# Kernel tuning notes

Hardware: AMD Instinct MI355X
Metric: run time of the kernel (lower is better)

## Reference

```python
import jax, jax.numpy as jnp
import numpy as np

D_MODEL = 1024
D_FF = 4096


def _layernorm(x, gamma, beta, eps=1e-5):
    mu = jnp.mean(x, axis=-1, keepdims=True)
    var = jnp.var(x, axis=-1, keepdims=True)
    return (x - mu) * jax.lax.rsqrt(var + eps) * gamma + beta


def setup_inputs() -> dict:
    key = jax.random.key(0)
    ks = jax.random.split(key, 7)
    B, S = 4, 2048
    src = jax.random.normal(ks[0], (B, S, D_MODEL), dtype=jnp.float32)
    gamma1 = jnp.ones((D_MODEL,), jnp.float32)
    beta1 = jnp.zeros((D_MODEL,), jnp.float32)
    gamma2 = jnp.ones((D_MODEL,), jnp.float32)
    beta2 = jnp.zeros((D_MODEL,), jnp.float32)
    w1 = jax.random.normal(ks[1], (D_MODEL, D_FF), jnp.float32) * (1.0 / np.sqrt(D_MODEL))
    b1 = jnp.zeros((D_FF,), jnp.float32)
    w2 = jax.random.normal(ks[2], (D_FF, D_MODEL), jnp.float32) * (1.0 / np.sqrt(D_FF))
    b2 = jnp.zeros((D_MODEL,), jnp.float32)
    return {"src": src, "gamma1": gamma1, "beta1": beta1,
            "gamma2": gamma2, "beta2": beta2,
            "w1": w1, "b1": b1, "w2": w2, "b2": b2}


def reference(src, gamma1, beta1, gamma2, beta2, w1, b1, w2, b2):
    # Pre-LN self-attention (single head, Q=K=V=norm_x, no projections)
    norm_x = _layernorm(src, gamma1, beta1)
    dim_k = norm_x.shape[-1]
    scores = jnp.einsum('bqd,bkd->bqk', norm_x, norm_x) / jnp.sqrt(jnp.float32(dim_k))
    weights = jax.nn.softmax(scores, axis=-1)
    attn = jnp.einsum('bqk,bkd->bqd', weights, norm_x)
    x = src + attn  # dropout p=0 -> identity
    # Pre-LN FFN
    h = _layernorm(x, gamma2, beta2)
    h = jax.nn.gelu(h @ w1 + b1, approximate=False)
    h = h @ w2 + b2
    return h + x
```

## Files before the change

### kernel.cpp

```cpp
#include <hip/hip_runtime.h>
#include <hip/hip_bf16.h>
#include <math.h>

typedef __attribute__((ext_vector_type(8))) short s8vec;
typedef __attribute__((ext_vector_type(16))) float f32x16;
typedef __attribute__((ext_vector_type(4))) unsigned short us4;

__device__ __forceinline__ unsigned short f2bf(float f) {
  unsigned u = __float_as_uint(f);
  u = (u + 0x7fffu + ((u >> 16) & 1u)) >> 16;
  return (unsigned short)u;
}
__device__ __forceinline__ float bf2f(unsigned short u) {
  return __uint_as_float(((unsigned)u) << 16);
}

__device__ __forceinline__ float fast_gelu(float t) {
  float t2 = t * t;
  float u = t * (1.59576912f + 0.07135481f * t2);
  float e = __expf(-u);
  return t * __frcp_rn(1.0f + e);
}

__device__ __forceinline__ void async_ld16(const unsigned short* g, unsigned short* l) {
  __builtin_amdgcn_global_load_lds(
      (__attribute__((address_space(1))) void*)g,
      (__attribute__((address_space(3))) void*)l, 16, 0, 0);
}

template <int EPI>
__global__ __launch_bounds__(256) void gemm_nt(
    const unsigned short* __restrict__ A, const unsigned short* __restrict__ B,
    float* __restrict__ outF, unsigned short* __restrict__ outB,
    const float* __restrict__ bias, const float* __restrict__ res,
    int M, int N, int K,
    long long bA, long long bB, long long bO, long long bR, float scale)
{
  __shared__ __align__(16) unsigned short As[128 * 64];
  __shared__ __align__(16) unsigned short Bs[128 * 64];

  const int tid = threadIdx.x;
  const int w = tid >> 6;
  const int l = tid & 63;
  const int z = blockIdx.z;

  A += (size_t)z * bA;
  B += (size_t)z * bB;

  const size_t tileM = (size_t)blockIdx.y * 128;
  const size_t tileN = (size_t)blockIdx.x * 128;

  const int sRow = l >> 3;
  const unsigned short* aP[4];
  const unsigned short* bP[4];
#pragma unroll
  for (int i = 0; i < 4; ++i) {
    const int c = (l & 7) ^ sRow ^ i;
    aP[i] = A + (tileM + (w << 5) + (i << 3) + sRow) * (size_t)K + (c << 3);
    bP[i] = B + (tileN + (w << 5) + (i << 3) + sRow) * (size_t)K + (c << 3);
  }
  unsigned short* ldsA = &As[(w << 5) * 64];
  unsigned short* ldsB = &Bs[(w << 5) * 64];

  const int wm = (w >> 1) << 6;
  const int wn = (w & 1) << 6;
  const int fr = l & 31;
  const int fq = l >> 5;
  const int swz = (l & 7) ^ ((l >> 3) & 3);
  const int aRow = (wm + fr) * 64;
  const int bRow = (wn + fr) * 64;

  f32x16 acc[2][2] = {};

  for (int k0 = 0; k0 < K; k0 += 64) {
    __syncthreads();
#pragma unroll
    for (int i = 0; i < 4; ++i) {
      async_ld16(aP[i] + k0, ldsA + (i << 3) * 64);
      async_ld16(bP[i] + k0, ldsB + (i << 3) * 64);
    }
    __syncthreads();

#pragma unroll
    for (int s = 0; s < 4; ++s) {
      const int p = ((s << 1) + fq) ^ swz;
      s8vec af[2], bf[2];
#pragma unroll
      for (int i = 0; i < 2; ++i)
        af[i] = *(const s8vec*)&As[aRow + (i << 11) + (p << 3)];
#pragma unroll
      for (int j = 0; j < 2; ++j)
        bf[j] = *(const s8vec*)&Bs[bRow + (j << 11) + (p << 3)];
#pragma unroll
      for (int i = 0; i < 2; ++i)
#pragma unroll
        for (int j = 0; j < 2; ++j)
          acc[i][j] = __builtin_amdgcn_mfma_f32_32x32x16_bf16(af[i], bf[j], acc[i][j], 0, 0, 0);
    }
  }

  float* oF = outF + (size_t)z * bO;
  unsigned short* oB = outB + (size_t)z * bO;
  const float* rs = res + (size_t)z * bR;

  float bcol[2];
  if (EPI >= 2) {
#pragma unroll
    for (int j = 0; j < 2; ++j) bcol[j] = bias[tileN + wn + (j << 5) + fr];
  }

#pragma unroll
  for (int i = 0; i < 2; ++i) {
#pragma unroll
    for (int r = 0; r < 16; ++r) {
      const size_t row = tileM + wm + (i << 5) + (r & 3) + ((r >> 2) << 3) + (fq << 2);
      const size_t rb = row * (size_t)N;
#pragma unroll
      for (int j = 0; j < 2; ++j) {
        const size_t col = tileN + wn + (j << 5) + fr;
        const float v = acc[i][j][r];
        if (EPI == 0) {
          oB[rb + col] = f2bf(v * scale);
        } else if (EPI == 1) {
          oF[rb + col] = v + rs[rb + col];
        } else if (EPI == 2) {
          oB[rb + col] = f2bf(fast_gelu(v + bcol[j]));
        } else {
          oF[rb + col] = v + bcol[j] + rs[rb + col];
        }
      }
    }
  }
}

__global__ __launch_bounds__(256) void ln_row(
    const float* __restrict__ x, const float* __restrict__ gamma,
    const float* __restrict__ beta, unsigned short* __restrict__ out)
{
  const int row = blockIdx.x;
  const float4* xr = (const float4*)(x + (size_t)row * 1024);
  const int tid = threadIdx.x;
  float4 v = xr[tid];
  float s = v.x + v.y + v.z + v.w;
  float q = v.x * v.x + v.y * v.y + v.z * v.z + v.w * v.w;
#pragma unroll
  for (int off = 32; off > 0; off >>= 1) {
    s += __shfl_down(s, off);
    q += __shfl_down(q, off);
  }
  __shared__ float rs_[4], rq_[4];
  const int w = tid >> 6, l = tid & 63;
  if (l == 0) { rs_[w] = s; rq_[w] = q; }
  __syncthreads();
  s = rs_[0] + rs_[1] + rs_[2] + rs_[3];
  q = rq_[0] + rq_[1] + rq_[2] + rq_[3];
  const float mu = s * (1.0f / 1024.0f);
  const float var = q * (1.0f / 1024.0f) - mu * mu;
  const float rstd = rsqrtf(var + 1e-5f);
  const float4 g = ((const float4*)gamma)[tid];
  const float4 b = ((const float4*)beta)[tid];
  us4 o;
  o.x = f2bf((v.x - mu) * rstd * g.x + b.x);
  o.y = f2bf((v.y - mu) * rstd * g.y + b.y);
  o.z = f2bf((v.z - mu) * rstd * g.z + b.z);
  o.w = f2bf((v.w - mu) * rstd * g.w + b.w);
  ((us4*)(out + (size_t)row * 1024))[tid] = o;
}

__global__ __launch_bounds__(256) void softmax_row(
    const unsigned short* __restrict__ sc, unsigned short* __restrict__ pr)
{
  const int row = blockIdx.x;
  const s8vec* s8 = (const s8vec*)(sc + (size_t)row * 2048);
  const int tid = threadIdx.x;
  s8vec a = s8[tid];
  float x[8];
#pragma unroll
  for (int i = 0; i < 8; ++i) x[i] = bf2f((unsigned short)a[i]);
  float mx = x[0];
#pragma unroll
  for (int i = 1; i < 8; ++i) mx = fmaxf(mx, x[i]);
#pragma unroll
  for (int off = 32; off > 0; off >>= 1) mx = fmaxf(mx, __shfl_down(mx, off));
  __shared__ float red[4];
  const int w = tid >> 6, l = tid & 63;
  if (l == 0) red[w] = mx;
  __syncthreads();
  mx = fmaxf(fmaxf(red[0], red[1]), fmaxf(red[2], red[3]));
  __syncthreads();
  float e[8], s = 0.f;
#pragma unroll
  for (int i = 0; i < 8; ++i) { e[i] = __expf(x[i] - mx); s += e[i]; }
#pragma unroll
  for (int off = 32; off > 0; off >>= 1) s += __shfl_down(s, off);
  if (l == 0) red[w] = s;
  __syncthreads();
  s = red[0] + red[1] + red[2] + red[3];
  const float inv = 1.0f / s;
  s8vec o;
#pragma unroll
  for (int i = 0; i < 8; ++i) o[i] = (short)f2bf(e[i] * inv);
  ((s8vec*)(pr + (size_t)row * 2048))[tid] = o;
}

template <bool BF16IN>
__global__ __launch_bounds__(256) void transpose_conv(
    const void* __restrict__ in_, unsigned short* __restrict__ out,
    int R, int C, long long bIn, long long bOut)
{
  __shared__ float tile[32][33];
  const int z = blockIdx.z;
  const int tx = threadIdx.x, ty = threadIdx.y;
  const int c0 = blockIdx.x * 32, r0 = blockIdx.y * 32;
  if (BF16IN) {
    const unsigned short* in = (const unsigned short*)in_ + (size_t)z * bIn;
    for (int i = ty; i < 32; i += 8)
      tile[i][tx] = bf2f(in[(size_t)(r0 + i) * C + c0 + tx]);
  } else {
    const float* in = (const float*)in_ + (size_t)z * bIn;
    for (int i = ty; i < 32; i += 8)
      tile[i][tx] = in[(size_t)(r0 + i) * C + c0 + tx];
  }
  __syncthreads();
  unsigned short* o = out + (size_t)z * bOut;
  for (int i = ty; i < 32; i += 8)
    o[(size_t)(c0 + i) * R + r0 + tx] = f2bf(tile[tx][i]);
}

extern "C" void kernel_launch(void* const* d_in, const int* in_sizes, int n_in,
                              void* d_out, int out_size, void* d_ws, size_t ws_size,
                              hipStream_t stream)
{
  (void)in_sizes; (void)n_in; (void)out_size; (void)ws_size;
  const float* src = (const float*)d_in[0];
  const float* g1  = (const float*)d_in[1];
  const float* be1 = (const float*)d_in[2];
  const float* g2  = (const float*)d_in[3];
  const float* be2 = (const float*)d_in[4];
  const float* w1  = (const float*)d_in[5];
  const float* b1  = (const float*)d_in[6];
  const float* w2  = (const float*)d_in[7];
  const float* b2  = (const float*)d_in[8];
  float* out = (float*)d_out;

  char* ws = (char*)d_ws;
  const size_t SZ_NORMX  = (size_t)8192 * 1024 * 2;
  const size_t SZ_SCORES = (size_t)4 * 2048 * 2048 * 4;
  const size_t SZ_PROBS  = (size_t)4 * 2048 * 2048 * 2;
  const size_t SZ_X      = (size_t)8192 * 1024 * 4;
  const size_t SZ_W1T    = (size_t)1024 * 4096 * 2;

  unsigned short* normx  = (unsigned short*)(ws);
  unsigned short* normxT = (unsigned short*)(ws + SZ_NORMX);
  unsigned short* scores = (unsigned short*)(ws + 2 * SZ_NORMX);
  unsigned short* probs  = (unsigned short*)(ws + 2 * SZ_NORMX + SZ_SCORES);
  float*          xbuf   = (float*)(ws + 2 * SZ_NORMX + SZ_SCORES + SZ_PROBS);
  unsigned short* w1t    = (unsigned short*)(ws + 2 * SZ_NORMX + SZ_SCORES + SZ_PROBS + SZ_X);
  unsigned short* w2t    = (unsigned short*)(ws + 2 * SZ_NORMX + SZ_SCORES + SZ_PROBS + SZ_X + SZ_W1T);
  unsigned short* normx2 = normx;
  unsigned short* hbuf   = scores;

  const dim3 tb(32, 8);
  transpose_conv<false><<<dim3(128, 32, 1), tb, 0, stream>>>(w1, w1t, 1024, 4096, 0, 0);
  transpose_conv<false><<<dim3(32, 128, 1), tb, 0, stream>>>(w2, w2t, 4096, 1024, 0, 0);

  ln_row<<<8192, 256, 0, stream>>>(src, g1, be1, normx);
  transpose_conv<true><<<dim3(32, 64, 4), tb, 0, stream>>>(
      normx, normxT, 2048, 1024, (long long)2048 * 1024, (long long)1024 * 2048);

  gemm_nt<0><<<dim3(16, 16, 4), 256, 0, stream>>>(
      normx, normx, nullptr, scores, nullptr, nullptr,
      2048, 2048, 1024,
      (long long)2048 * 1024, (long long)2048 * 1024, (long long)2048 * 2048, 0, 0.03125f);

  softmax_row<<<8192, 256, 0, stream>>>(scores, probs);

  gemm_nt<1><<<dim3(8, 16, 4), 256, 0, stream>>>(
      probs, normxT, xbuf, nullptr, nullptr, src,
      2048, 1024, 2048,
      (long long)2048 * 2048, (long long)1024 * 2048, (long long)2048 * 1024,
      (long long)2048 * 1024, 1.0f);

  ln_row<<<8192, 256, 0, stream>>>(xbuf, g2, be2, normx2);

  gemm_nt<2><<<dim3(32, 64, 1), 256, 0, stream>>>(
      normx2, w1t, nullptr, hbuf, b1, nullptr,
      8192, 4096, 1024, 0, 0, 0, 0, 1.0f);

  gemm_nt<3><<<dim3(8, 64, 1), 256, 0, stream>>>(
      hbuf, w2t, out, nullptr, b2, xbuf,
      8192, 1024, 4096, 0, 0, 0, 0, 1.0f);
}
```

Baseline: 432.7 us.

## Replace GEMM with 256-row tile, 8-wave double-buffered pipelined kernel

```diff
diff --git a/kernel.cpp b/kernel.cpp
--- a/kernel.cpp
+++ b/kernel.cpp
@@ -28,105 +28,178 @@
       (__attribute__((address_space(3))) void*)l, 16, 0, 0);
 }
 
-template <int EPI>
-__global__ __launch_bounds__(256) void gemm_nt(
+
+#define STA(q, tk, bofs) async_ld16(srcA[q] + ((size_t)(tk) << 6), &As[(bofs) + ldsA[q]])
+#define STB(j, tk, bofs) async_ld16(srcB[j] + ((size_t)(tk) << 6), &Bs[(bofs) + ldsB[j]])
+
+#define ARD(Q)                                                              \
+  _Pragma("unroll") for (int s = 0; s < 4; ++s)                             \
+      af[s] = *(const s8vec*)&As[aB + aoff + (Q)*2048 + pc[s]];
+
+#define MFMA_PH(Q)                                                          \
+  __builtin_amdgcn_s_barrier();                                             \
+  asm volatile("s_waitcnt lgkmcnt(0)" ::: "memory");                        \
+  __builtin_amdgcn_sched_barrier(0);                                        \
+  __builtin_amdgcn_s_setprio(1);                                            \
+  _Pragma("unroll") for (int s = 0; s < 4; ++s) {                           \
+    _Pragma("unroll") for (int nf = 0; nf < NF; ++nf)                       \
+      acc[Q][nf] = __builtin_amdgcn_mfma_f32_32x32x16_bf16(                 \
+          af[s], b[nf][s], acc[Q][nf], 0, 0, 0);                            \
+  }                                                                         \
+  __builtin_amdgcn_s_setprio(0);
+
+template <int BN, int EPI>
+__global__ __launch_bounds__(512, 2) void gemm_nt8(
     const unsigned short* __restrict__ A, const unsigned short* __restrict__ B,
     float* __restrict__ outF, unsigned short* __restrict__ outB,
     const float* __restrict__ bias, const float* __restrict__ res,
     int M, int N, int K,
     long long bA, long long bB, long long bO, long long bR, float scale)
 {
-  __shared__ __align__(16) unsigned short As[128 * 64];
-  __shared__ __align__(16) unsigned short Bs[128 * 64];
-
+  static_assert(BN == 256 || BN == 128, "BN must be 256 or 128");
+  constexpr int NB = BN / 64;
+  constexpr int NF = BN / 128;
+  constexpr int WN = BN / 4;
+  constexpr int ABUF = 256 * 64;
+  constexpr int BBUF = BN * 64;
+
+  __shared__ __align__(16) unsigned short As[2 * ABUF];
+  __shared__ __align__(16) unsigned short Bs[2 * BBUF];
+
+  (void)M;
   const int tid = threadIdx.x;
   const int w = tid >> 6;
   const int l = tid & 63;
   const int z = blockIdx.z;
-
   A += (size_t)z * bA;
   B += (size_t)z * bB;
-
-  const size_t tileM = (size_t)blockIdx.y * 128;
-  const size_t tileN = (size_t)blockIdx.x * 128;
-
-  const int sRow = l >> 3;
-  const unsigned short* aP[4];
-  const unsigned short* bP[4];
-#pragma unroll
-  for (int i = 0; i < 4; ++i) {
-    const int c = (l & 7) ^ sRow ^ i;
-    aP[i] = A + (tileM + (w << 5) + (i << 3) + sRow) * (size_t)K + (c << 3);
-    bP[i] = B + (tileN + (w << 5) + (i << 3) + sRow) * (size_t)K + (c << 3);
-  }
-  unsigned short* ldsA = &As[(w << 5) * 64];
-  unsigned short* ldsB = &Bs[(w << 5) * 64];
-
-  const int wm = (w >> 1) << 6;
-  const int wn = (w & 1) << 6;
+  const size_t tileM = (size_t)blockIdx.y * 256;
+  const size_t tileN = (size_t)blockIdx.x * BN;
+
+  const int sub = w & 3, half = w >> 2;
+  const unsigned short* srcA[4];
+  int ldsA[4];
+#pragma unroll
+  for (int q = 0; q < 4; ++q) {
+    const int rb = q * 32 + sub * 8 + half * 128;
+    const int r = rb + (l >> 3);
+    const int c = (l & 7) ^ (r & 7) ^ ((r >> 3) & 3);
+    srcA[q] = A + (tileM + r) * (size_t)K + (c << 3);
+    ldsA[q] = rb * 64;
+  }
+  const unsigned short* srcB[NB];
+  int ldsB[NB];
+#pragma unroll
+  for (int j = 0; j < NB; ++j) {
+    const int rb = j * 64 + w * 8;
+    const int r = rb + (l >> 3);
+    const int c = (l & 7) ^ (r & 7) ^ ((r >> 3) & 3);
+    srcB[j] = B + (tileN + r) * (size_t)K + (c << 3);
+    ldsB[j] = rb * 64;
+  }
+
+  const int wm = half;
+  const int wn = sub;
   const int fr = l & 31;
   const int fq = l >> 5;
   const int swz = (l & 7) ^ ((l >> 3) & 3);
-  const int aRow = (wm + fr) * 64;
-  const int bRow = (wn + fr) * 64;
-
-  f32x16 acc[2][2] = {};
-
-  for (int k0 = 0; k0 < K; k0 += 64) {
-    __syncthreads();
-#pragma unroll
-    for (int i = 0; i < 4; ++i) {
-      async_ld16(aP[i] + k0, ldsA + (i << 3) * 64);
-      async_ld16(bP[i] + k0, ldsB + (i << 3) * 64);
+  int pc[4];
+#pragma unroll
+  for (int s = 0; s < 4; ++s) pc[s] = ((((s << 1) + fq) ^ swz) << 3);
+  const int aoff = (wm * 128 + fr) * 64;
+  int boff[NF];
+#pragma unroll
+  for (int nf = 0; nf < NF; ++nf) boff[nf] = (wn * WN + nf * 32 + fr) * 64;
+
+  f32x16 acc[4][NF] = {};
+  const int NT = K >> 6;
+
+  STA(0, 0, 0); STA(1, 0, 0); STA(2, 0, 0); STA(3, 0, 0);
+#pragma unroll
+  for (int j = 0; j < NB; ++j) STB(j, 0, 0);
+#pragma unroll
+  for (int j = 0; j < NB; ++j) STB(j, 1, BBUF);
+  STA(0, 1, ABUF); STA(1, 1, ABUF);
+  if constexpr (BN == 256) asm volatile("s_waitcnt vmcnt(6)" ::: "memory");
+  else                     asm volatile("s_waitcnt vmcnt(4)" ::: "memory");
+  __builtin_amdgcn_s_barrier();
+
+  auto tile = [&](int t, int bf) {
+    const int aB = bf * ABUF;
+    const int bBo = bf * BBUF;
+    const int oaB = (bf ^ 1) * ABUF;
+    const bool g1 = (t + 1 < NT), g2 = (t + 2 < NT);
+    s8vec b[NF][4];
+    s8vec af[4];
+
+    ARD(0);
+#pragma unroll
+    for (int nf = 0; nf < NF; ++nf)
+#pragma unroll
+      for (int s = 0; s < 4; ++s)
+        b[nf][s] = *(const s8vec*)&Bs[bBo + boff[nf] + pc[s]];
+    if (g1) { STA(2, t + 1, oaB); STA(3, t + 1, oaB); }
+    MFMA_PH(0);
+    __builtin_amdgcn_s_barrier();
+
+    ARD(1);
+    if (g2) {
+      if constexpr (BN == 256) { STB(0, t + 2, bBo); STB(1, t + 2, bBo); }
+      else                     { STB(0, t + 2, bBo); }
     }
-    __syncthreads();
-
-#pragma unroll
-    for (int s = 0; s < 4; ++s) {
-      const int p = ((s << 1) + fq) ^ swz;
-      s8vec af[2], bf[2];
-#pragma unroll
-      for (int i = 0; i < 2; ++i)
-        af[i] = *(const s8vec*)&As[aRow + (i << 11) + (p << 3)];
-#pragma unroll
-      for (int j = 0; j < 2; ++j)
-        bf[j] = *(const s8vec*)&Bs[bRow + (j << 11) + (p << 3)];
-#pragma unroll
-      for (int i = 0; i < 2; ++i)
-#pragma unroll
-        for (int j = 0; j < 2; ++j)
-          acc[i][j] = __builtin_amdgcn_mfma_f32_32x32x16_bf16(af[i], bf[j], acc[i][j], 0, 0, 0);
+    MFMA_PH(1);
+    __builtin_amdgcn_s_barrier();
+
+    ARD(2);
+    if (g2) {
+      if constexpr (BN == 256) { STB(2, t + 2, bBo); STB(3, t + 2, bBo); }
+      else                     { STB(1, t + 2, bBo); }
     }
-  }
+    MFMA_PH(2);
+    __builtin_amdgcn_s_barrier();
+
+    ARD(3);
+    if (g2) { STA(0, t + 2, aB); STA(1, t + 2, aB); }
+    MFMA_PH(3);
+    if (g2) {
+      if constexpr (BN == 256) asm volatile("s_waitcnt vmcnt(6)" ::: "memory");
+      else                     asm volatile("s_waitcnt vmcnt(4)" ::: "memory");
+    } else {
+      asm volatile("s_waitcnt vmcnt(0)" ::: "memory");
+    }
+    __builtin_amdgcn_s_barrier();
+  };
+
+  for (int t = 0; t < NT; t += 2) { tile(t, 0); tile(t + 1, 1); }
 
   float* oF = outF + (size_t)z * bO;
   unsigned short* oB = outB + (size_t)z * bO;
   const float* rs = res + (size_t)z * bR;
 
-  float bcol[2];
+  float bcol[NF];
   if (EPI >= 2) {
 #pragma unroll
-    for (int j = 0; j < 2; ++j) bcol[j] = bias[tileN + wn + (j << 5) + fr];
-  }
-
-#pragma unroll
-  for (int i = 0; i < 2; ++i) {
+    for (int nf = 0; nf < NF; ++nf) bcol[nf] = bias[tileN + wn * WN + nf * 32 + fr];
+  }
+
+#pragma unroll
+  for (int mf = 0; mf < 4; ++mf) {
 #pragma unroll
     for (int r = 0; r < 16; ++r) {
-      const size_t row = tileM + wm + (i << 5) + (r & 3) + ((r >> 2) << 3) + (fq << 2);
+      const size_t row = tileM + wm * 128 + (mf << 5) + (r & 3) + ((r >> 2) << 3) + (fq << 2);
       const size_t rb = row * (size_t)N;
 #pragma unroll
-      for (int j = 0; j < 2; ++j) {
-        const size_t col = tileN + wn + (j << 5) + fr;
-        const float v = acc[i][j][r];
+      for (int nf = 0; nf < NF; ++nf) {
+        const size_t col = tileN + wn * WN + (nf << 5) + fr;
+        const float v = acc[mf][nf][r];
         if (EPI == 0) {
           oB[rb + col] = f2bf(v * scale);
         } else if (EPI == 1) {
           oF[rb + col] = v + rs[rb + col];
         } else if (EPI == 2) {
-          oB[rb + col] = f2bf(fast_gelu(v + bcol[j]));
+          oB[rb + col] = f2bf(fast_gelu(v + bcol[nf]));
         } else {
-          oF[rb + col] = v + bcol[j] + rs[rb + col];
+          oF[rb + col] = v + bcol[nf] + rs[rb + col];
         }
       }
     }
@@ -268,14 +341,14 @@
   transpose_conv<true><<<dim3(32, 64, 4), tb, 0, stream>>>(
       normx, normxT, 2048, 1024, (long long)2048 * 1024, (long long)1024 * 2048);
 
-  gemm_nt<0><<<dim3(16, 16, 4), 256, 0, stream>>>(
+  gemm_nt8<256, 0><<<dim3(8, 8, 4), 512, 0, stream>>>(
       normx, normx, nullptr, scores, nullptr, nullptr,
       2048, 2048, 1024,
       (long long)2048 * 1024, (long long)2048 * 1024, (long long)2048 * 2048, 0, 0.03125f);
 
   softmax_row<<<8192, 256, 0, stream>>>(scores, probs);
 
-  gemm_nt<1><<<dim3(8, 16, 4), 256, 0, stream>>>(
+  gemm_nt8<128, 1><<<dim3(8, 8, 4), 512, 0, stream>>>(
       probs, normxT, xbuf, nullptr, nullptr, src,
       2048, 1024, 2048,
       (long long)2048 * 2048, (long long)1024 * 2048, (long long)2048 * 1024,
@@ -283,11 +356,11 @@
 
   ln_row<<<8192, 256, 0, stream>>>(xbuf, g2, be2, normx2);
 
-  gemm_nt<2><<<dim3(32, 64, 1), 256, 0, stream>>>(
+  gemm_nt8<256, 2><<<dim3(16, 32, 1), 512, 0, stream>>>(
       normx2, w1t, nullptr, hbuf, b1, nullptr,
       8192, 4096, 1024, 0, 0, 0, 0, 1.0f);
 
-  gemm_nt<3><<<dim3(8, 64, 1), 256, 0, stream>>>(
+  gemm_nt8<128, 3><<<dim3(8, 32, 1), 512, 0, stream>>>(
       hbuf, w2t, out, nullptr, b2, xbuf,
       8192, 1024, 4096, 0, 0, 0, 0, 1.0f);
 }
```

After: 429.3 us. Within noise of the previous version (-0.8%).
